# Performance work log

Hardware: AMD Instinct MI355X
Metric: run time of the kernel (lower is better)

Reference implementation:

```python
import jax, jax.numpy as jnp
import numpy as np

# Static config (from set_param of the wrapped deformable conv)
N, CIN, H, W = 8, 64, 128, 128
COUT, KH, KW = 64, 3, 3
STRIDE, PAD, DIL = 1, 1, 1
WEIGHT_BIT = 8
K = KH * KW
HO = (H + 2 * PAD - DIL * (KH - 1) - 1) // STRIDE + 1
WO = (W + 2 * PAD - DIL * (KW - 1) - 1) // STRIDE + 1


def setup_inputs() -> dict:
    key = jax.random.key(0)
    k1, k2, k3 = jax.random.split(key, 3)
    x = jax.random.normal(k1, (N, CIN, H, W), dtype=jnp.float32)
    offset = jax.random.normal(k2, (N, 2 * K, HO, WO), dtype=jnp.float32)
    weight = jax.random.normal(k3, (COUT, CIN, KH, KW), dtype=jnp.float32) * 0.05
    return {"x": x, "offset": offset, "weight": weight}


def quantize_weight_symmetric(w, bits):
    # HAWQ/CoDeNet symmetric per-tensor quant: scale = max(|min|,|max|)/n,
    # q = clamp(round(w/scale), -n-1, n) * scale, straight-through estimator.
    n = 2 ** (bits - 1) - 1
    sat = jnp.maximum(jnp.abs(w.min()), jnp.abs(w.max()))
    scale = jnp.maximum(sat, 1e-8) / n
    wq = jnp.clip(jnp.round(w / scale), -n - 1, n) * scale
    return w + jax.lax.stop_gradient(wq - w)


def deform_conv2d(x, offset, weight):
    # x: [N,C,H,W]; offset: [N, 2*K, HO, WO] (y,x interleaved per kernel tap)
    # Base sampling grid for each kernel tap and output location.
    ky, kx = jnp.meshgrid(jnp.arange(KH), jnp.arange(KW), indexing='ij')
    ky = ky.reshape(K).astype(jnp.float32)  # [K]
    kx = kx.reshape(K).astype(jnp.float32)
    ho = jnp.arange(HO, dtype=jnp.float32)
    wo = jnp.arange(WO, dtype=jnp.float32)
    base_y = ho[None, :, None] * STRIDE - PAD + ky[:, None, None] * DIL  # [K,HO,1]
    base_x = wo[None, None, :] * STRIDE - PAD + kx[:, None, None] * DIL  # [K,1,WO]

    off = offset.reshape(N, K, 2, HO, WO)
    py = base_y[None] + off[:, :, 0]  # [N,K,HO,WO]
    px = base_x[None] + off[:, :, 1]

    y0 = jnp.floor(py)
    x0 = jnp.floor(px)
    dy = py - y0
    dx = px - x0
    y0i = y0.astype(jnp.int32)
    x0i = x0.astype(jnp.int32)

    xf = x.reshape(N, CIN, H * W)

    def gather_corner(yi, xi, wgt):
        # zero padding outside the image
        valid = (yi >= 0) & (yi < H) & (xi >= 0) & (xi < W)
        idx = jnp.clip(yi, 0, H - 1) * W + jnp.clip(xi, 0, W - 1)  # [N,K,HO,WO]
        vals = jax.vmap(lambda xn, idn: xn[:, idn.reshape(-1)])(xf, idx)
        vals = vals.reshape(N, CIN, K, HO, WO)
        return vals * (wgt * valid.astype(wgt.dtype))[:, None]  # [N,1,K,HO,WO]

    sampled = (
        gather_corner(y0i, x0i, (1.0 - dy) * (1.0 - dx))
        + gather_corner(y0i, x0i + 1, (1.0 - dy) * dx)
        + gather_corner(y0i + 1, x0i, dy * (1.0 - dx))
        + gather_corner(y0i + 1, x0i + 1, dy * dx)
    )  # [N,CIN,K,HO,WO]

    out = jnp.einsum('nckhw,ock->nohw', sampled, weight.reshape(COUT, CIN, K))
    return out


def reference(x, offset, weight):
    wq = quantize_weight_symmetric(weight, WEIGHT_BIT)
    return deform_conv2d(x, offset, wq)
```

## Files before the change

### kernel.cpp

```cpp
#include <hip/hip_runtime.h>
#include <hip/hip_bf16.h>

#define NB    8
#define CCH   64
#define HH    128
#define WW    128
#define KTAP  9
#define HW    (HH * WW)
#define KSTEPS 18
#define NW    36864

typedef _Float16 f16x8 __attribute__((ext_vector_type(8)));
typedef _Float16 f16x2 __attribute__((ext_vector_type(2)));
typedef __attribute__((ext_vector_type(4))) float f32x4;

__device__ inline unsigned int pack_f16(float a, float b) {
    f16x2 h;
    h[0] = (_Float16)a;
    h[1] = (_Float16)b;
    return __builtin_bit_cast(unsigned int, h);
}

__device__ inline f16x8 as_f16x8(uint4 u) { return __builtin_bit_cast(f16x8, u); }

__device__ inline void lds_barrier() {
    asm volatile("s_waitcnt lgkmcnt(0)\n\ts_barrier" ::: "memory");
}

__global__ __launch_bounds__(256) void prep_kernel(const float* __restrict__ x,
                                                   const float* __restrict__ w,
                                                   unsigned int* __restrict__ xt32,
                                                   uint4* __restrict__ bq) {
    __shared__ float tile[64 * 65];
    const int t = threadIdx.x;
    const int bid = blockIdx.x;

    if (bid < 2048) {
        const int n = bid >> 8;
        const int pbase = (bid & 255) * 64;
        #pragma unroll
        for (int i = 0; i < 4; i++) {
            int idx = i * 256 + t;
            int c = idx >> 4, f4 = idx & 15;
            float4 v = *(const float4*)&x[((size_t)(n * CCH + c)) * HW + pbase + f4 * 4];
            float* d = &tile[c * 65 + f4 * 4];
            d[0] = v.x; d[1] = v.y; d[2] = v.z; d[3] = v.w;
        }
        __syncthreads();
        const int px = t >> 2, c4 = t & 3;
        float f[16];
        #pragma unroll
        for (int j = 0; j < 16; j++) f[j] = tile[(c4 * 16 + j) * 65 + px];
        unsigned int o8[8];
        #pragma unroll
        for (int i = 0; i < 8; i++) o8[i] = pack_f16(f[2 * i], f[2 * i + 1]);
        uint4* dst = (uint4*)&xt32[((size_t)(n * HW + pbase + px)) * 32 + c4 * 8];
        dst[0] = make_uint4(o8[0], o8[1], o8[2], o8[3]);
        dst[1] = make_uint4(o8[4], o8[5], o8[6], o8[7]);
    } else {
        float m0 = 0.f, m1 = 0.f, m2 = 0.f, m3 = 0.f;
        for (int i = t; i < NW; i += 1024) {
            m0 = fmaxf(m0, fabsf(w[i]));
            m1 = fmaxf(m1, fabsf(w[i + 256]));
            m2 = fmaxf(m2, fabsf(w[i + 512]));
            m3 = fmaxf(m3, fabsf(w[i + 768]));
        }
        float m = fmaxf(fmaxf(m0, m1), fmaxf(m2, m3));
        #pragma unroll
        for (int off = 32; off > 0; off >>= 1)
            m = fmaxf(m, __shfl_down(m, off));
        if ((t & 63) == 0) tile[t >> 6] = m;
        __syncthreads();
        m = fmaxf(fmaxf(tile[0], tile[1]), fmaxf(tile[2], tile[3]));
        const float scale = fmaxf(m, 1e-8f) / 127.f;
        const float inv_scale = 1.f / scale;

        const int rec = (bid - 2048) * 256 + t;
        int nt  = rec / (KSTEPS * 64);
        int rem = rec - nt * (KSTEPS * 64);
        int s    = rem >> 6;
        int lane = rem & 63;
        int quad = lane >> 4, n16 = lane & 15;
        int o = nt * 16 + n16;
        unsigned int u[4];
        #pragma unroll
        for (int jj = 0; jj < 4; jj++) {
            float q[2];
            #pragma unroll
            for (int h = 0; h < 2; h++) {
                int k   = s * 32 + quad * 8 + 2 * jj + h;
                int c   = k & 63;
                int tap = k >> 6;
                float v  = w[(o * CCH + c) * KTAP + tap];
                float qq = rintf(v * inv_scale);
                q[h] = fminf(fmaxf(qq, -128.f), 127.f) * scale;
            }
            u[jj] = pack_f16(q[0], q[1]);
        }
        bq[rec] = make_uint4(u[0], u[1], u[2], u[3]);
    }
}

__global__ __launch_bounds__(256) void deform_mfma(const unsigned short* __restrict__ xt,
                                                   const float* __restrict__ offset,
                                                   const uint4* __restrict__ bq,
                                                   float* __restrict__ out) {
    __shared__ __align__(16) _Float16 Abuf[2][4096];
    __shared__ unsigned int SC[576];
    __shared__ uint2 SW[576];

    const int t    = threadIdx.x;
    const int wid  = t >> 6;
    const int lane = t & 63;
    const int quad = lane >> 4, n16 = lane & 15;
    const int bid  = blockIdx.x;
    const int n    = bid & 7;
    const int px0  = (bid >> 3) * 64;
    const int pg   = t >> 3;
    const int q8   = t & 7;

    const char* xb = (const char*)(xt + (size_t)n * HW * CCH);
    const float* offn = offset + (size_t)n * 2 * KTAP * HW;

    for (int u = t; u < 576; u += 256) {
        const int tap = u >> 6, p = u & 63;
        const int ppx = px0 + p;
        const int ho = ppx >> 7, wo = ppx & 127;
        const int ky = tap / 3, kx = tap - 3 * ky;
        const float py  = (float)(ho - 1 + ky) + offn[(2 * tap) * HW + ppx];
        const float pxf = (float)(wo - 1 + kx) + offn[(2 * tap + 1) * HW + ppx];
        const float fy = floorf(py), fx = floorf(pxf);
        const int y0 = (int)fy, x0 = (int)fx;
        const float dy = py - fy, dx = pxf - fx;
        const int y1 = y0 + 1, x1 = x0 + 1;
        const bool vy0 = (y0 >= 0) && (y0 < HH);
        const bool vy1 = (y1 >= 0) && (y1 < HH);
        const bool vx0 = (x0 >= 0) && (x0 < WW);
        const bool vx1 = (x1 >= 0) && (x1 < WW);
        const int y0c = min(max(y0, 0), HH - 1);
        const int y1c = min(max(y1, 0), HH - 1);
        const int x0c = min(max(x0, 0), WW - 1);
        const int x1c = min(max(x1, 0), WW - 1);
        const float w00 = (1.f - dy) * (1.f - dx) * ((vy0 && vx0) ? 1.f : 0.f);
        const float w01 = (1.f - dy) * dx         * ((vy0 && vx1) ? 1.f : 0.f);
        const float w10 = dy * (1.f - dx)         * ((vy1 && vx0) ? 1.f : 0.f);
        const float w11 = dy * dx                 * ((vy1 && vx1) ? 1.f : 0.f);
        SC[u] = (unsigned)(y0c | (x0c << 7) | (y1c << 14) | (x1c << 21));
        SW[u] = make_uint2(pack_f16(w00, w01), pack_f16(w10, w11));
    }
    __syncthreads();

    f32x4 acc[4];
    #pragma unroll
    for (int mt = 0; mt < 4; mt++) acc[mt] = (f32x4){0.f, 0.f, 0.f, 0.f};

    uint4 rset[8];
    uint4 bset[2][2];

    auto issue_stage = [&](int s) {
        #pragma unroll
        for (int r = 0; r < 2; r++) {
            const int p = pg + 32 * r;
            const unsigned int cc = SC[s * 64 + p];
            const int y0b = (int)(cc & 127) << 14;
            const int x0b = (int)((cc >> 7) & 127) << 7;
            const int y1b = (int)((cc >> 14) & 127) << 14;
            const int x1b = (int)(cc >> 21) << 7;
            const char* base = xb + q8 * 16;
            rset[4 * r + 0] = *(const uint4*)(base + (y0b | x0b));
            rset[4 * r + 1] = *(const uint4*)(base + (y0b | x1b));
            rset[4 * r + 2] = *(const uint4*)(base + (y1b | x0b));
            rset[4 * r + 3] = *(const uint4*)(base + (y1b | x1b));
        }
        bset[s & 1][0] = bq[((size_t)wid * KSTEPS + 2 * s) * 64 + lane];
        bset[s & 1][1] = bq[((size_t)wid * KSTEPS + 2 * s + 1) * 64 + lane];
    };
    auto blend_stage = [&](int s) {
        _Float16* dst = Abuf[s & 1];
        #pragma unroll
        for (int r = 0; r < 2; r++) {
            const int p = pg + 32 * r;
            const uint2 ww = SW[s * 64 + p];
            const f16x2 wA = __builtin_bit_cast(f16x2, ww.x);
            const f16x2 wB = __builtin_bit_cast(f16x2, ww.y);
            f16x8 sa = as_f16x8(rset[4 * r + 0]) * wA[0];
            sa += as_f16x8(rset[4 * r + 1]) * wA[1];
            sa += as_f16x8(rset[4 * r + 2]) * wB[0];
            sa += as_f16x8(rset[4 * r + 3]) * wB[1];
            *(f16x8*)&dst[p * 64 + ((q8 ^ (p & 7)) * 8)] = sa;
        }
    };
    auto mma_stage = [&](int s) {
        const _Float16* sub = Abuf[s & 1];
        #pragma unroll
        for (int ks = 0; ks < 2; ks++) {
            const f16x8 bf = __builtin_bit_cast(f16x8, bset[s & 1][ks]);
            const int slot = (ks * 4 + quad) ^ (n16 & 7);
            #pragma unroll
            for (int mt = 0; mt < 4; mt++) {
                const int rr = mt * 16 + n16;
                const f16x8 a = *(const f16x8*)&sub[rr * 64 + slot * 8];
                acc[mt] = __builtin_amdgcn_mfma_f32_16x16x32_f16(a, bf, acc[mt], 0, 0, 0);
            }
        }
    };

    issue_stage(0);
    #pragma unroll
    for (int s = 0; s < 9; s++) {
        blend_stage(s);
        if (s < 8) issue_stage(s + 1);
        lds_barrier();
        mma_stage(s);
    }

    const int o = wid * 16 + n16;
    #pragma unroll
    for (int mt = 0; mt < 4; mt++) {
        float4 v = make_float4(acc[mt].x, acc[mt].y, acc[mt].z, acc[mt].w);
        float* dst = out + ((size_t)(n * CCH + o)) * HW + px0 + mt * 16 + quad * 4;
        *(float4*)dst = v;
    }
}

extern "C" void kernel_launch(void* const* d_in, const int* in_sizes, int n_in,
                              void* d_out, int out_size, void* d_ws, size_t ws_size,
                              hipStream_t stream) {
    const float* x      = (const float*)d_in[0];
    const float* offset = (const float*)d_in[1];
    const float* weight = (const float*)d_in[2];
    float* out = (float*)d_out;

    unsigned char* ws = (unsigned char*)d_ws;
    uint4*        bq   = (uint4*)ws;
    unsigned int* xt32 = (unsigned int*)(ws + 131072);
    const unsigned short* xt = (const unsigned short*)xt32;

    prep_kernel<<<2048 + 18, 256, 0, stream>>>(x, weight, xt32, bq);
    deform_mfma<<<2048, 256, 0, stream>>>(xt, offset, bq, out);
}
```

Baseline: 130.8 us.

## Drop gather register prefetch and double buffer to raise occupancy

Removes the register-held prefetch of the next stage's bilinear corner loads and the double-buffered LDS A tile. Gathers are now issued and blended in the same stage, with an extra barrier per step protecting the single buffer. The launch bound asks for 8 blocks per SM to cut register and LDS pressure, relying on more resident waves to hide gather latency. In exchange it gives up intra-wave overlap of loads with MFMA and adds a synchronization point every step.

Measured after the change: 132.1 us. No clear change (+0.9%).

```diff
diff --git a/kernel.cpp b/kernel.cpp
--- a/kernel.cpp
+++ b/kernel.cpp
@@ -101,11 +101,11 @@
     }
 }
 
-__global__ __launch_bounds__(256) void deform_mfma(const unsigned short* __restrict__ xt,
-                                                   const float* __restrict__ offset,
-                                                   const uint4* __restrict__ bq,
-                                                   float* __restrict__ out) {
-    __shared__ __align__(16) _Float16 Abuf[2][4096];
+__global__ __launch_bounds__(256, 8) void deform_mfma(const unsigned short* __restrict__ xt,
+                                                      const float* __restrict__ offset,
+                                                      const uint4* __restrict__ bq,
+                                                      float* __restrict__ out) {
+    __shared__ __align__(16) _Float16 Abuf[4096];
     __shared__ unsigned int SC[576];
     __shared__ uint2 SW[576];
 
@@ -154,44 +154,33 @@
     #pragma unroll
     for (int mt = 0; mt < 4; mt++) acc[mt] = (f32x4){0.f, 0.f, 0.f, 0.f};
 
-    uint4 rset[8];
     uint4 bset[2][2];
 
-    auto issue_stage = [&](int s) {
-        #pragma unroll
-        for (int r = 0; r < 2; r++) {
-            const int p = pg + 32 * r;
+    auto blend_stage = [&](int s) {
+        #pragma unroll
+        for (int rr = 0; rr < 2; rr++) {
+            const int p = pg + 32 * rr;
             const unsigned int cc = SC[s * 64 + p];
+            const uint2 wwp = SW[s * 64 + p];
             const int y0b = (int)(cc & 127) << 14;
             const int x0b = (int)((cc >> 7) & 127) << 7;
             const int y1b = (int)((cc >> 14) & 127) << 14;
             const int x1b = (int)(cc >> 21) << 7;
             const char* base = xb + q8 * 16;
-            rset[4 * r + 0] = *(const uint4*)(base + (y0b | x0b));
-            rset[4 * r + 1] = *(const uint4*)(base + (y0b | x1b));
-            rset[4 * r + 2] = *(const uint4*)(base + (y1b | x0b));
-            rset[4 * r + 3] = *(const uint4*)(base + (y1b | x1b));
-        }
-        bset[s & 1][0] = bq[((size_t)wid * KSTEPS + 2 * s) * 64 + lane];
-        bset[s & 1][1] = bq[((size_t)wid * KSTEPS + 2 * s + 1) * 64 + lane];
-    };
-    auto blend_stage = [&](int s) {
-        _Float16* dst = Abuf[s & 1];
-        #pragma unroll
-        for (int r = 0; r < 2; r++) {
-            const int p = pg + 32 * r;
-            const uint2 ww = SW[s * 64 + p];
-            const f16x2 wA = __builtin_bit_cast(f16x2, ww.x);
-            const f16x2 wB = __builtin_bit_cast(f16x2, ww.y);
-            f16x8 sa = as_f16x8(rset[4 * r + 0]) * wA[0];
-            sa += as_f16x8(rset[4 * r + 1]) * wA[1];
-            sa += as_f16x8(rset[4 * r + 2]) * wB[0];
-            sa += as_f16x8(rset[4 * r + 3]) * wB[1];
-            *(f16x8*)&dst[p * 64 + ((q8 ^ (p & 7)) * 8)] = sa;
+            const uint4 c00 = *(const uint4*)(base + (y0b | x0b));
+            const uint4 c01 = *(const uint4*)(base + (y0b | x1b));
+            const uint4 c10 = *(const uint4*)(base + (y1b | x0b));
+            const uint4 c11 = *(const uint4*)(base + (y1b | x1b));
+            const f16x2 wA = __builtin_bit_cast(f16x2, wwp.x);
+            const f16x2 wB = __builtin_bit_cast(f16x2, wwp.y);
+            f16x8 sa = as_f16x8(c00) * wA[0];
+            sa += as_f16x8(c01) * wA[1];
+            sa += as_f16x8(c10) * wB[0];
+            sa += as_f16x8(c11) * wB[1];
+            *(f16x8*)&Abuf[p * 64 + ((q8 ^ (p & 7)) * 8)] = sa;
         }
     };
     auto mma_stage = [&](int s) {
-        const _Float16* sub = Abuf[s & 1];
         #pragma unroll
         for (int ks = 0; ks < 2; ks++) {
             const f16x8 bf = __builtin_bit_cast(f16x8, bset[s & 1][ks]);
@@ -199,19 +188,25 @@
             #pragma unroll
             for (int mt = 0; mt < 4; mt++) {
                 const int rr = mt * 16 + n16;
-                const f16x8 a = *(const f16x8*)&sub[rr * 64 + slot * 8];
+                const f16x8 a = *(const f16x8*)&Abuf[rr * 64 + slot * 8];
                 acc[mt] = __builtin_amdgcn_mfma_f32_16x16x32_f16(a, bf, acc[mt], 0, 0, 0);
             }
         }
     };
 
-    issue_stage(0);
+    bset[0][0] = bq[((size_t)wid * KSTEPS + 0) * 64 + lane];
+    bset[0][1] = bq[((size_t)wid * KSTEPS + 1) * 64 + lane];
+
     #pragma unroll
     for (int s = 0; s < 9; s++) {
         blend_stage(s);
-        if (s < 8) issue_stage(s + 1);
+        if (s < 8) {
+            bset[(s + 1) & 1][0] = bq[((size_t)wid * KSTEPS + 2 * (s + 1)) * 64 + lane];
+            bset[(s + 1) & 1][1] = bq[((size_t)wid * KSTEPS + 2 * (s + 1) + 1) * 64 + lane];
+        }
         lds_barrier();
         mma_stage(s);
+        lds_barrier();
     }
 
     const int o = wid * 16 + n16;
```
